# Kernel tuning notes

Measured on AMD Instinct MI355X. Metric: run time of the kernel, lower is better.

## Reference

```python
import jax, jax.numpy as jnp
import numpy as np

NUM_HEADS = 8
EPS = 1e-12  # torch F.normalize eps


def setup_inputs() -> dict:
    key = jax.random.key(0)
    k1, k2, k3 = jax.random.split(key, 3)
    B, N, C = 8, 4096, 768
    x = jax.random.normal(k1, (B, N, C), dtype=jnp.float32)
    Wqkv = jax.random.normal(k2, (C, 3 * C), dtype=jnp.float32) * 0.02
    temperature = jnp.ones((NUM_HEADS, 1, 1), dtype=jnp.float32)
    Wproj = jax.random.normal(k3, (C, C), dtype=jnp.float32) * 0.02
    bproj = jnp.zeros((C,), dtype=jnp.float32)
    return {"x": x, "Wqkv": Wqkv, "temperature": temperature,
            "Wproj": Wproj, "bproj": bproj}


def _l2norm(t):
    # torch F.normalize(dim=-1): x / max(||x||, eps)
    n = jnp.sqrt(jnp.sum(t * t, axis=-1, keepdims=True))
    return t / jnp.maximum(n, EPS)


def reference(x, Wqkv, temperature, Wproj, bproj):
    B, N, C = x.shape
    H = NUM_HEADS
    Ch = C // H
    qkv = (x @ Wqkv).reshape(B, N, 3, H, Ch)
    qkv = qkv.transpose(2, 0, 3, 1, 4)           # (3, B, H, N, Ch)
    q, k, v = qkv[0], qkv[1], qkv[2]
    # transpose(-2,-1): attend over channels -> (B, H, Ch, N)
    q = jnp.swapaxes(q, -2, -1)
    k = jnp.swapaxes(k, -2, -1)
    v = jnp.swapaxes(v, -2, -1)
    q = _l2norm(q)
    k = _l2norm(k)
    # (B, H, Ch, Ch) channel-attention scores, scaled by learned temperature
    attn = jnp.einsum('bhcn,bhdn->bhcd', q, k) * temperature
    attn = jax.nn.softmax(attn, axis=-1)
    out = jnp.einsum('bhcd,bhdn->bhcn', attn, v)  # (B, H, Ch, N)
    out = out.transpose(0, 3, 1, 2).reshape(B, N, C)
    return out @ Wproj + bproj
```

## Files before the change

kernel.cpp:

```cpp
#include <hip/hip_runtime.h>
#include <cstdint>
#include <cstddef>

typedef unsigned short u16;
typedef short bf16x8 __attribute__((ext_vector_type(8)));
typedef unsigned short u16x4 __attribute__((ext_vector_type(4)));
typedef unsigned short u16x8 __attribute__((ext_vector_type(8)));
typedef float f32x4 __attribute__((ext_vector_type(4)));

#define EPSN 1e-12f

__device__ __forceinline__ u16 f2bf(float f) {
  uint32_t u = __builtin_bit_cast(uint32_t, f);
  u += 0x7FFFu + ((u >> 16) & 1u);
  return (u16)(u >> 16);
}
__device__ __forceinline__ float bf2f(u16 h) {
  uint32_t u = ((uint32_t)h) << 16;
  return __builtin_bit_cast(float, u);
}

__device__ __forceinline__ void gll16(const u16* g, u16* l) {
  __builtin_amdgcn_global_load_lds(
      (const __attribute__((address_space(1))) void*)g,
      (__attribute__((address_space(3))) void*)l, 16, 0, 0);
}

__global__ __launch_bounds__(256)
void k_cvtT(const float* __restrict__ x, u16* __restrict__ Xh,
            u16* __restrict__ XhT) {
  __shared__ u16 tr[64][68];
  const int tid = threadIdx.x;
  const int t0 = blockIdx.x * 64, k0 = blockIdx.y * 64, b = blockIdx.z;
  const size_t base = ((size_t)b * 4096 + t0) * 768 + k0;
#pragma unroll
  for (int p = 0; p < 4; p++) {
    const int r = (tid >> 4) + p * 16;
    const int c = (tid & 15) * 4;
    f32x4 v = *(const f32x4*)(x + base + (size_t)r * 768 + c);
    u16x4 o;
#pragma unroll
    for (int e = 0; e < 4; e++) o[e] = f2bf(v[e]);
    *(u16x4*)(Xh + base + (size_t)r * 768 + c) = o;
    tr[c + 0][r] = o[0];
    tr[c + 1][r] = o[1];
    tr[c + 2][r] = o[2];
    tr[c + 3][r] = o[3];
  }
  __syncthreads();
  const size_t tbase = ((size_t)b * 768 + k0) * 4096 + t0;
#pragma unroll
  for (int p = 0; p < 4; p++) {
    const int kk = (tid >> 4) + p * 16;
    const int ts = (tid & 15) * 4;
    u16x4 o;
#pragma unroll
    for (int e = 0; e < 4; e++) o[e] = tr[kk][ts + e];
    *(u16x4*)(XhT + tbase + (size_t)kk * 4096 + ts) = o;
  }
}

__global__ __launch_bounds__(256)
void k_wt(const float* __restrict__ W, u16* __restrict__ Wt, u16* __restrict__ Wvh) {
  __shared__ float tile[32][33];
  const int j0 = blockIdx.x * 32;
  const int k0 = blockIdx.y * 32;
  const int tx = threadIdx.x & 31;
  const int ty = threadIdx.x >> 5;
#pragma unroll
  for (int r = 0; r < 4; r++) {
    float v = W[(size_t)(k0 + ty + r * 8) * 2304 + j0 + tx];
    tile[ty + r * 8][tx] = v;
    if (j0 >= 1536)
      Wvh[(size_t)(k0 + ty + r * 8) * 768 + (j0 - 1536) + tx] = f2bf(v);
  }
  __syncthreads();
  if (j0 < 1536) {
#pragma unroll
    for (int r = 0; r < 4; r++)
      Wt[(size_t)(j0 + ty + r * 8) * 768 + k0 + tx] = f2bf(tile[tx][ty + r * 8]);
  }
}

template <int OUTF32B>
__global__ __launch_bounds__(256, 3)
void k_gemm(const u16* __restrict__ A, const u16* __restrict__ Btp,
            void* __restrict__ Cp, const float* __restrict__ bias,
            int K, int lda, int ldb, int ldc,
            long aZ, long bZ, long cZ, int zK, long kss) {
  __shared__ u16 As[128 * 32];
  __shared__ u16 Bs[128 * 32];
  const int tid = threadIdx.x;
  const int lane = tid & 63;
  const int wid = tid >> 6;
  const int wr = wid >> 1, wc = wid & 1;
  const int fm = lane & 15, kg = lane >> 4;
  const int m0 = blockIdx.y * 128;
  const int n0 = blockIdx.x * 128;
  const int z = blockIdx.z;
  const int bb = z / zK, ss = z % zK;
  const u16* Az = A + (long)bb * aZ + (long)ss * kss;
  const u16* Btz = Btp + (long)bb * bZ + (long)ss * kss;

  const int lr = lane >> 2;
  const int gk = (lane & 3) ^ ((lane >> 3) & 3);
  const u16* gA0 = Az + (size_t)(m0 + wid * 32 + lr) * lda + gk * 8;
  const u16* gA1 = gA0 + (size_t)16 * lda;
  const u16* gB0 = Btz + (size_t)(n0 + wid * 32 + lr) * ldb + gk * 8;
  const u16* gB1 = gB0 + (size_t)16 * ldb;
  u16* lA0 = As + wid * 1024;
  u16* lA1 = lA0 + 512;
  u16* lB0 = Bs + wid * 1024;
  u16* lB1 = lB0 + 512;
  const int kq = (kg ^ ((fm >> 1) & 3)) * 8;

  f32x4 acc[4][4] = {};
  for (int k0 = 0; k0 < K; k0 += 32) {
    __syncthreads();
    gll16(gA0, lA0);
    gll16(gA1, lA1);
    gll16(gB0, lB0);
    gll16(gB1, lB1);
    gA0 += 32; gA1 += 32; gB0 += 32; gB1 += 32;
    __syncthreads();
    bf16x8 af[4], bfr[4];
#pragma unroll
    for (int i = 0; i < 4; i++)
      af[i] = *(const bf16x8*)&As[(wr * 64 + i * 16 + fm) * 32 + kq];
#pragma unroll
    for (int j = 0; j < 4; j++)
      bfr[j] = *(const bf16x8*)&Bs[(wc * 64 + j * 16 + fm) * 32 + kq];
#pragma unroll
    for (int i = 0; i < 4; i++)
#pragma unroll
      for (int j = 0; j < 4; j++)
        acc[i][j] = __builtin_amdgcn_mfma_f32_16x16x32_bf16(af[i], bfr[j], acc[i][j], 0, 0, 0);
  }

  if constexpr (OUTF32B) {
    float* C = (float*)Cp + (long)z * cZ;
#pragma unroll
    for (int j = 0; j < 4; j++) {
      const int col = n0 + wc * 64 + j * 16 + fm;
      const float bj = bias[col];
#pragma unroll
      for (int i = 0; i < 4; i++) {
        const int r0 = m0 + wr * 64 + i * 16 + kg * 4;
#pragma unroll
        for (int r = 0; r < 4; r++)
          C[(size_t)(r0 + r) * ldc + col] = acc[i][j][r] + bj;
      }
    }
  } else {
    u16* C = (u16*)Cp + (long)z * cZ;
#pragma unroll
    for (int j = 0; j < 4; j++) {
      const int col = n0 + wc * 64 + j * 16 + fm;
#pragma unroll
      for (int i = 0; i < 4; i++) {
        const int r0 = m0 + wr * 64 + i * 16 + kg * 4;
#pragma unroll
        for (int r = 0; r < 4; r++)
          C[(size_t)(r0 + r) * ldc + col] = f2bf(acc[i][j][r]);
      }
    }
  }
}

__global__ __launch_bounds__(256)
void k_red(const u16* __restrict__ P, u16* __restrict__ O) {
  const int b = blockIdx.y;
  const size_t r = ((size_t)blockIdx.x * 256 + threadIdx.x) * 8;
  const u16* p = P + (size_t)b * 4 * 589824 + r;
  u16x8 v0 = *(const u16x8*)(p);
  u16x8 v1 = *(const u16x8*)(p + 589824);
  u16x8 v2 = *(const u16x8*)(p + 2 * 589824);
  u16x8 v3 = *(const u16x8*)(p + 3 * 589824);
  u16x8 o;
#pragma unroll
  for (int e = 0; e < 8; e++)
    o[e] = f2bf(bf2f(v0[e]) + bf2f(v1[e]) + bf2f(v2[e]) + bf2f(v3[e]));
  *(u16x8*)(O + (size_t)b * 589824 + r) = o;
}

__global__ __launch_bounds__(256)
void k_score(const u16* __restrict__ Tm, const u16* __restrict__ Wt,
             const float* __restrict__ temperature, float* __restrict__ Aattn) {
  const int h = blockIdx.x, b = blockIdx.y;
  const int bh = b * 8 + h;
  __shared__ u16 As[96 * 32];
  __shared__ u16 Bs[96 * 32];
  __shared__ u16 Dt2[96 * 32];
  __shared__ u16 Dwq[96 * 32];
  __shared__ float Gs[96 * 96];
  __shared__ float nqs[96], nks[96], invk[96];

  const int tid = threadIdx.x;
  const int lane = tid & 63;
  const int wid = tid >> 6;
  const int wr = wid >> 1, wc = wid & 1;
  const int fm = lane & 15, kg = lane >> 4;
  const int lr = lane >> 2;
  const int gkS = (lane & 3) ^ ((lane >> 3) & 3);
  const int gkL = (lane & 3);
  const int kq = (kg ^ ((fm >> 1) & 3)) * 8;

  const u16* baseT1 = Tm + (size_t)b * 1179648 + (size_t)(h * 96) * 768;
  const u16* baseT2 = baseT1 + (size_t)768 * 768;
  const u16* baseWq = Wt + (size_t)(h * 96) * 768;
  const u16* baseWk = baseWq + (size_t)768 * 768;

  const u16* gsrc;
  u16* ldst;
  int gblk = gkS;
  if (wid == 0) { gsrc = baseT1; ldst = As; }
  else if (wid == 1) { gsrc = baseWk; ldst = Bs; }
  else if (wid == 2) { gsrc = baseT2; ldst = Dt2; gblk = gkL; }
  else { gsrc = baseWq; ldst = Dwq; gblk = gkL; }

  f32x4 acc[3][3] = {};
  float nqa = 0.f, nka = 0.f;
  const int sw1 = (tid < 96) ? ((tid >> 1) & 3) : 0;
  const int sw2 = (tid >= 128 && tid < 224) ? (((tid - 128) >> 1) & 3) : 0;

  for (int k0 = 0; k0 < 768; k0 += 32) {
    __syncthreads();
#pragma unroll
    for (int c = 0; c < 6; c++) {
      gll16(gsrc + (size_t)(c * 16 + lr) * 768 + k0 + gblk * 8,
            ldst + c * 512);
    }
    __syncthreads();
    bf16x8 af[3], bfr[3];
#pragma unroll
    for (int i = 0; i < 3; i++)
      af[i] = *(const bf16x8*)&As[(wr * 48 + i * 16 + fm) * 32 + kq];
#pragma unroll
    for (int j = 0; j < 3; j++)
      bfr[j] = *(const bf16x8*)&Bs[(wc * 48 + j * 16 + fm) * 32 + kq];
#pragma unroll
    for (int i = 0; i < 3; i++)
#pragma unroll
      for (int j = 0; j < 3; j++)
        acc[i][j] = __builtin_amdgcn_mfma_f32_16x16x32_bf16(af[i], bfr[j], acc[i][j], 0, 0, 0);
    if (tid < 96) {
#pragma unroll
      for (int g = 0; g < 4; g++) {
        u16x8 a = *(const u16x8*)&As[tid * 32 + (g ^ sw1) * 8];
        u16x8 w = *(const u16x8*)&Dwq[tid * 32 + g * 8];
#pragma unroll
        for (int e = 0; e < 8; e++) nqa += bf2f(a[e]) * bf2f(w[e]);
      }
    } else if (tid >= 128 && tid < 224) {
      const int d = tid - 128;
#pragma unroll
      for (int g = 0; g < 4; g++) {
        u16x8 a = *(const u16x8*)&Bs[d * 32 + (g ^ sw2) * 8];
        u16x8 w = *(const u16x8*)&Dt2[d * 32 + g * 8];
#pragma unroll
        for (int e = 0; e < 8; e++) nka += bf2f(a[e]) * bf2f(w[e]);
      }
    }
  }

  if (tid < 96) nqs[tid] = nqa;
  if (tid >= 128 && tid < 224) nks[tid - 128] = nka;
#pragma unroll
  for (int i = 0; i < 3; i++)
#pragma unroll
    for (int j = 0; j < 3; j++)
#pragma unroll
      for (int r = 0; r < 4; r++)
        Gs[(wr * 48 + i * 16 + kg * 4 + r) * 96 + wc * 48 + j * 16 + fm] = acc[i][j][r];
  __syncthreads();
  if (tid < 96) invk[tid] = 1.0f / fmaxf(sqrtf(nks[tid]), EPSN);
  __syncthreads();
  if (tid < 96) {
    const int c = tid;
    const float iq = temperature[h] / fmaxf(sqrtf(nqs[c]), EPSN);
    float sv[96];
    float m = -1e30f;
#pragma unroll
    for (int d = 0; d < 96; d++) {
      float s = Gs[c * 96 + d] * iq * invk[d];
      sv[d] = s;
      m = fmaxf(m, s);
    }
    float sum = 0.f;
#pragma unroll
    for (int d = 0; d < 96; d++) {
      float e = __expf(sv[d] - m);
      sv[d] = e;
      sum += e;
    }
    const float inv = 1.0f / sum;
    float* dst = Aattn + (size_t)bh * 9216 + (size_t)c * 96;
#pragma unroll
    for (int d = 0; d < 96; d++) dst[d] = sv[d] * inv;
  }
}

__global__ __launch_bounds__(256)
void k_weff(const float* __restrict__ Aattn, const float* __restrict__ Wproj,
            u16* __restrict__ Weff) {
  const int jt = blockIdx.x, h = blockIdx.y, b = blockIdx.z;
  const int bh = b * 8 + h;
  __shared__ float As2[9216];
  const int tid = threadIdx.x;
  for (int idx = tid; idx < 9216; idx += 256)
    As2[idx] = Aattn[(size_t)bh * 9216 + idx];
  __syncthreads();
  const int jloc = tid & 127;
  const int half = tid >> 7;
  const int j = jt * 128 + jloc;
  float acc[48] = {};
  for (int c = 0; c < 96; c++) {
    const float w = Wproj[(size_t)(h * 96 + c) * 768 + j];
    const f32x4* ar = (const f32x4*)&As2[c * 96 + half * 48];
#pragma unroll
    for (int v4 = 0; v4 < 12; v4++) {
      f32x4 a = ar[v4];
      acc[v4 * 4 + 0] += w * a[0];
      acc[v4 * 4 + 1] += w * a[1];
      acc[v4 * 4 + 2] += w * a[2];
      acc[v4 * 4 + 3] += w * a[3];
    }
  }
  u16* dst = Weff + ((size_t)b * 768 + j) * 768 + h * 96 + half * 48;
#pragma unroll
  for (int v4 = 0; v4 < 12; v4++) {
    u16x4 o;
    o[0] = f2bf(acc[v4 * 4 + 0]);
    o[1] = f2bf(acc[v4 * 4 + 1]);
    o[2] = f2bf(acc[v4 * 4 + 2]);
    o[3] = f2bf(acc[v4 * 4 + 3]);
    *(u16x4*)(dst + v4 * 4) = o;
  }
}

extern "C" void kernel_launch(void* const* d_in, const int* in_sizes, int n_in,
                              void* d_out, int out_size, void* d_ws, size_t ws_size,
                              hipStream_t stream) {
  const float* x = (const float*)d_in[0];
  const float* Wqkv = (const float*)d_in[1];
  const float* temp = (const float*)d_in[2];
  const float* Wproj = (const float*)d_in[3];
  const float* bproj = (const float*)d_in[4];
  float* out = (float*)d_out;

  char* ws = (char*)d_ws;
  u16* Xh = (u16*)ws;
  u16* XhT = (u16*)(ws + 50331648);
  u16* Wt = (u16*)(ws + 100663296);
  u16* Wvh = (u16*)(ws + 103022592);
  u16* XtXp = (u16*)(ws + 104202240);
  u16* XtXbf = (u16*)(ws + 141950976);
  u16* T = (u16*)(ws + 151388160);
  u16* WeffT = (u16*)(ws + 151388160);
  u16* WcompT = (u16*)(ws + 160825344);
  float* Aattn = (float*)(ws + 170262528);

  k_cvtT<<<dim3(64, 12, 8), 256, 0, stream>>>(x, Xh, XhT);
  k_wt<<<dim3(72, 24), 256, 0, stream>>>(Wqkv, Wt, Wvh);
  k_gemm<0><<<dim3(6, 6, 32), 256, 0, stream>>>(
      XhT, XhT, (void*)XtXp, nullptr, 1024, 4096, 4096, 768,
      3145728L, 3145728L, 589824L, 4, 1024L);
  k_red<<<dim3(288, 8), 256, 0, stream>>>(XtXp, XtXbf);
  k_gemm<0><<<dim3(6, 12, 8), 256, 0, stream>>>(
      Wt, XtXbf, (void*)T, nullptr, 768, 768, 768, 768,
      0L, 589824L, 1179648L, 1, 0L);
  k_score<<<dim3(8, 8), 256, 0, stream>>>(T, Wt, temp, Aattn);
  k_weff<<<dim3(6, 8, 8), 256, 0, stream>>>(Aattn, Wproj, WeffT);
  k_gemm<0><<<dim3(6, 6, 8), 256, 0, stream>>>(
      WeffT, Wvh, (void*)WcompT, nullptr, 768, 768, 768, 768,
      589824L, 0L, 589824L, 1, 0L);
  k_gemm<1><<<dim3(6, 32, 8), 256, 0, stream>>>(
      Xh, WcompT, out, bproj, 768, 768, 768, 768,
      3145728L, 589824L, 3145728L, 1, 0L);
}
```

Measured before the change: 307.3 us.

## Exploit symmetry of XᵀX Gram to compute only upper-triangular tiles; add XCD block remap

The split-K Gram GEMM now computes only the 21 upper-triangular 128x128 tiles instead of all 36, writing them as packed tiles. The reduction kernel sums the four split-K partials per tile through LDS and mirrors them (transposed) to fill the lower triangle. All GEMM launches also remap block IDs so consecutive work goes to the same XCD, aiming at better L2 locality. The transposed LDS read in the mirror path may cause bank conflicts, and the reduction now uses far fewer blocks with heavy per-thread register accumulators.

```diff
diff --git a/kernel.cpp b/kernel.cpp
--- a/kernel.cpp
+++ b/kernel.cpp
@@ -82,12 +82,39 @@
   }
 }
 
-template <int OUTF32B>
+template <int OUTF32B, int TRI>
 __global__ __launch_bounds__(256, 3)
 void k_gemm(const u16* __restrict__ A, const u16* __restrict__ Btp,
             void* __restrict__ Cp, const float* __restrict__ bias,
             int K, int lda, int ldb, int ldc,
             long aZ, long bZ, long cZ, int zK, long kss) {
+  const int gx = gridDim.x, gy = gridDim.y;
+  int f = blockIdx.x + gx * (blockIdx.y + gy * blockIdx.z);
+  const int total = gx * gy * gridDim.z;
+  const int q = total >> 3, rr = total & 7;
+  const int xcd = f & 7, kk0 = f >> 3;
+  f = (xcd < rr ? xcd * (q + 1) : rr * (q + 1) + (xcd - rr) * q) + kk0;
+  const int bx = f % gx;
+  const int tmp = f / gx;
+  const int by = tmp % gy;
+  const int bz = tmp / gy;
+
+  int m0, n0;
+  if constexpr (TRI) {
+    const int ty = (bx >= 20) ? 5 : (bx >= 18) ? 4 : (bx >= 15) ? 3
+                 : (bx >= 11) ? 2 : (bx >= 6) ? 1 : 0;
+    const int txi = ty + (bx - (ty * 6 - (ty * (ty - 1)) / 2));
+    m0 = ty * 128;
+    n0 = txi * 128;
+  } else {
+    m0 = by * 128;
+    n0 = bx * 128;
+  }
+  const int z = bz;
+  const int bb = z / zK, ss = z % zK;
+  const u16* Az = A + (long)bb * aZ + (long)ss * kss;
+  const u16* Btz = Btp + (long)bb * bZ + (long)ss * kss;
+
   __shared__ u16 As[128 * 32];
   __shared__ u16 Bs[128 * 32];
   const int tid = threadIdx.x;
@@ -95,12 +122,6 @@
   const int wid = tid >> 6;
   const int wr = wid >> 1, wc = wid & 1;
   const int fm = lane & 15, kg = lane >> 4;
-  const int m0 = blockIdx.y * 128;
-  const int n0 = blockIdx.x * 128;
-  const int z = blockIdx.z;
-  const int bb = z / zK, ss = z % zK;
-  const u16* Az = A + (long)bb * aZ + (long)ss * kss;
-  const u16* Btz = Btp + (long)bb * bZ + (long)ss * kss;
 
   const int lr = lane >> 2;
   const int gk = (lane & 3) ^ ((lane >> 3) & 3);
@@ -152,16 +173,19 @@
       }
     }
   } else {
-    u16* C = (u16*)Cp + (long)z * cZ;
+    const int rb = TRI ? 0 : m0;
+    const int cb = TRI ? 0 : n0;
+    const int ld = TRI ? 128 : ldc;
+    u16* C = (u16*)Cp + (long)z * cZ + (TRI ? (long)bx * 16384 : 0L);
 #pragma unroll
     for (int j = 0; j < 4; j++) {
-      const int col = n0 + wc * 64 + j * 16 + fm;
+      const int col = cb + wc * 64 + j * 16 + fm;
 #pragma unroll
       for (int i = 0; i < 4; i++) {
-        const int r0 = m0 + wr * 64 + i * 16 + kg * 4;
+        const int r0 = rb + wr * 64 + i * 16 + kg * 4;
 #pragma unroll
         for (int r = 0; r < 4; r++)
-          C[(size_t)(r0 + r) * ldc + col] = f2bf(acc[i][j][r]);
+          C[(size_t)(r0 + r) * ld + col] = f2bf(acc[i][j][r]);
       }
     }
   }
@@ -170,17 +194,41 @@
 __global__ __launch_bounds__(256)
 void k_red(const u16* __restrict__ P, u16* __restrict__ O) {
   const int b = blockIdx.y;
-  const size_t r = ((size_t)blockIdx.x * 256 + threadIdx.x) * 8;
-  const u16* p = P + (size_t)b * 4 * 589824 + r;
-  u16x8 v0 = *(const u16x8*)(p);
-  u16x8 v1 = *(const u16x8*)(p + 589824);
-  u16x8 v2 = *(const u16x8*)(p + 2 * 589824);
-  u16x8 v3 = *(const u16x8*)(p + 3 * 589824);
-  u16x8 o;
-#pragma unroll
-  for (int e = 0; e < 8; e++)
-    o[e] = f2bf(bf2f(v0[e]) + bf2f(v1[e]) + bf2f(v2[e]) + bf2f(v3[e]));
-  *(u16x8*)(O + (size_t)b * 589824 + r) = o;
+  const int ti = blockIdx.x / 6, tj = blockIdx.x % 6;
+  const bool mirror = ti > tj;
+  const int a = mirror ? tj : ti;
+  const int c2 = mirror ? ti : tj;
+  const int src = a * 6 - (a * (a - 1)) / 2 + (c2 - a);
+  __shared__ u16 lt[128 * 128];
+  const int tid = threadIdx.x;
+  const int r = tid >> 1;
+  const int ch = (tid & 1) * 64;
+  float acc[64] = {};
+  for (int s = 0; s < 4; s++) {
+    const u16* p = P + ((size_t)(b * 4 + s) * 344064 + (size_t)src * 16384);
+    __syncthreads();
+#pragma unroll
+    for (int it = 0; it < 8; it++) {
+      const int idx = (tid + it * 256) * 8;
+      *(u16x8*)&lt[idx] = *(const u16x8*)(p + idx);
+    }
+    __syncthreads();
+    if (!mirror) {
+#pragma unroll
+      for (int e = 0; e < 64; e++) acc[e] += bf2f(lt[r * 128 + ch + e]);
+    } else {
+#pragma unroll
+      for (int e = 0; e < 64; e++) acc[e] += bf2f(lt[(ch + e) * 128 + r]);
+    }
+  }
+  u16* o = O + (size_t)b * 589824 + (size_t)(ti * 128 + r) * 768 + tj * 128 + ch;
+#pragma unroll
+  for (int v8 = 0; v8 < 8; v8++) {
+    u16x8 w;
+#pragma unroll
+    for (int e = 0; e < 8; e++) w[e] = f2bf(acc[v8 * 8 + e]);
+    *(u16x8*)(o + v8 * 8) = w;
+  }
 }
 
 __global__ __launch_bounds__(256)
@@ -246,19 +294,19 @@
     if (tid < 96) {
 #pragma unroll
       for (int g = 0; g < 4; g++) {
-        u16x8 a = *(const u16x8*)&As[tid * 32 + (g ^ sw1) * 8];
+        u16x8 av = *(const u16x8*)&As[tid * 32 + (g ^ sw1) * 8];
         u16x8 w = *(const u16x8*)&Dwq[tid * 32 + g * 8];
 #pragma unroll
-        for (int e = 0; e < 8; e++) nqa += bf2f(a[e]) * bf2f(w[e]);
+        for (int e = 0; e < 8; e++) nqa += bf2f(av[e]) * bf2f(w[e]);
       }
     } else if (tid >= 128 && tid < 224) {
       const int d = tid - 128;
 #pragma unroll
       for (int g = 0; g < 4; g++) {
-        u16x8 a = *(const u16x8*)&Bs[d * 32 + (g ^ sw2) * 8];
+        u16x8 av = *(const u16x8*)&Bs[d * 32 + (g ^ sw2) * 8];
         u16x8 w = *(const u16x8*)&Dt2[d * 32 + g * 8];
 #pragma unroll
-        for (int e = 0; e < 8; e++) nka += bf2f(a[e]) * bf2f(w[e]);
+        for (int e = 0; e < 8; e++) nka += bf2f(av[e]) * bf2f(w[e]);
       }
     }
   }
@@ -319,11 +367,11 @@
     const f32x4* ar = (const f32x4*)&As2[c * 96 + half * 48];
 #pragma unroll
     for (int v4 = 0; v4 < 12; v4++) {
-      f32x4 a = ar[v4];
-      acc[v4 * 4 + 0] += w * a[0];
-      acc[v4 * 4 + 1] += w * a[1];
-      acc[v4 * 4 + 2] += w * a[2];
-      acc[v4 * 4 + 3] += w * a[3];
+      f32x4 av = ar[v4];
+      acc[v4 * 4 + 0] += w * av[0];
+      acc[v4 * 4 + 1] += w * av[1];
+      acc[v4 * 4 + 2] += w * av[2];
+      acc[v4 * 4 + 3] += w * av[3];
     }
   }
   u16* dst = Weff + ((size_t)b * 768 + j) * 768 + h * 96 + half * 48;
@@ -362,19 +410,19 @@
 
   k_cvtT<<<dim3(64, 12, 8), 256, 0, stream>>>(x, Xh, XhT);
   k_wt<<<dim3(72, 24), 256, 0, stream>>>(Wqkv, Wt, Wvh);
-  k_gemm<0><<<dim3(6, 6, 32), 256, 0, stream>>>(
-      XhT, XhT, (void*)XtXp, nullptr, 1024, 4096, 4096, 768,
-      3145728L, 3145728L, 589824L, 4, 1024L);
-  k_red<<<dim3(288, 8), 256, 0, stream>>>(XtXp, XtXbf);
-  k_gemm<0><<<dim3(6, 12, 8), 256, 0, stream>>>(
+  k_gemm<0, 1><<<dim3(21, 1, 32), 256, 0, stream>>>(
+      XhT, XhT, (void*)XtXp, nullptr, 1024, 4096, 4096, 0,
+      3145728L, 3145728L, 344064L, 4, 1024L);
+  k_red<<<dim3(36, 8), 256, 0, stream>>>(XtXp, XtXbf);
+  k_gemm<0, 0><<<dim3(6, 12, 8), 256, 0, stream>>>(
       Wt, XtXbf, (void*)T, nullptr, 768, 768, 768, 768,
       0L, 589824L, 1179648L, 1, 0L);
   k_score<<<dim3(8, 8), 256, 0, stream>>>(T, Wt, temp, Aattn);
   k_weff<<<dim3(6, 8, 8), 256, 0, stream>>>(Aattn, Wproj, WeffT);
-  k_gemm<0><<<dim3(6, 6, 8), 256, 0, stream>>>(
+  k_gemm<0, 0><<<dim3(6, 6, 8), 256, 0, stream>>>(
       WeffT, Wvh, (void*)WcompT, nullptr, 768, 768, 768, 768,
       589824L, 0L, 589824L, 1, 0L);
-  k_gemm<1><<<dim3(6, 32, 8), 256, 0, stream>>>(
+  k_gemm<1, 0><<<dim3(6, 32, 8), 256, 0, stream>>>(
       Xh, WcompT, out, bproj, 768, 768, 768, 768,
       3145728L, 589824L, 3145728L, 1, 0L);
 }
```

Measured after the change: 304.5 us. Within noise of the previous version (-0.9%).
